# Performance work log

Measured on AMD Instinct MI355X. Metric: run time of the kernel, lower is better.

The kernel has to match this reference:

```python
import jax, jax.numpy as jnp
import numpy as np

N, E, C, EMB, NB, L = 20000, 640000, 64, 32, 8, 2
MAX_RADIUS = 2.5
NUM_NEIGHBORS = 32.0
RH = 32  # radial MLP hidden


def setup_inputs() -> dict:
    key = jax.random.key(0)
    ks = jax.random.split(key, 24)
    g = lambda k, shape, fan: (jax.random.normal(k, shape, dtype=jnp.float32) / np.sqrt(fan).astype(np.float32))
    inp = {
        'x': jax.random.normal(ks[0], (N, 6), dtype=jnp.float32),
        'batch': jnp.zeros((N,), dtype=jnp.int64),
        'node_attr': jax.random.randint(ks[1], (N,), 0, 100),
        'edge_src': jax.random.randint(ks[2], (E,), 0, N),
        'edge_dst': jax.random.randint(ks[3], (E,), 0, N),
        'emb_table': jax.random.normal(ks[4], (100, EMB), dtype=jnp.float32),
        'uplift_M': jax.random.normal(ks[5], (C, 2), dtype=jnp.float32),
        'h': jnp.ones((L,), jnp.float32) * 0.01,
        'mix': jnp.ones((L,), jnp.float32) * 0.5,
        'rad_W1': g(ks[6], (L, NB, RH), NB),
        'rad_b1': jnp.zeros((L, RH), jnp.float32),
        'rad_W2': g(ks[7], (L, RH, 2 * C), RH),
        'lin1_s': g(ks[8], (L, C, C), C),
        'lin1_v': g(ks[9], (L, C, C), C),
        'lin2_s': g(ks[10], (L, C, 2 * C), C),
        'lin2_v': g(ks[11], (L, C, C), C),
        'sc_s_w': g(ks[12], (L, C, EMB, 2 * C), C * EMB),
        'sc_v_w': g(ks[13], (L, C, EMB, C), C * EMB),
        'si_s': g(ks[14], (L, C, C), C),
        'si_v': g(ks[15], (L, C, C), C),
    }
    return inp


def _forward(x, batch, node_attr, edge_src, edge_dst, emb_table, uplift_M, h, mix,
             rad_W1, rad_b1, rad_W2, lin1_s, lin1_v, lin2_s, lin2_v,
             sc_s_w, sc_v_w, si_s, si_v):
    n = x.shape[0]
    emb = emb_table[node_attr]                       # [N, EMB] node embedding
    # semi-unitarize uplift matrix: Q = M (M^T M)^{-1/2} == U V^T
    U, _, Vt = jnp.linalg.svd(uplift_M, full_matrices=False)
    Q = U @ Vt                                       # [C, 2]
    xv = x.reshape(n, 2, 3)
    y_s = jnp.zeros((n, C), x.dtype)                 # hidden scalars start at 0
    y_v = jnp.einsum('nkx,ck->ncx', xv, Q)           # uplift vectors [N,C,3]
    y = (y_s, y_v)
    y_old = y
    nbas = jnp.arange(1, NB + 1, dtype=x.dtype)
    inv_nn = 1.0 / np.sqrt(NUM_NEIGHBORS).astype(np.float32)
    for i in range(L):
        pos = x[:, :3]
        ev = pos[edge_src] - pos[edge_dst]           # [E,3]
        elen = jnp.linalg.norm(ev, axis=1)
        safe = jnp.maximum(elen, 1e-9)
        sh = np.float32(np.sqrt(3.0)) * ev / safe[:, None]   # 1x1o SH, component norm
        # bessel radial basis, scaled by sqrt(NB)
        ef = (np.float32(np.sqrt(2.0 / MAX_RADIUS)) *
              jnp.sin(nbas[None, :] * jnp.pi * safe[:, None] / MAX_RADIUS) / safe[:, None])
        ef = ef * np.float32(np.sqrt(NB))
        # smooth cutoff (e3nn tetris style)
        u = 2.0 * (elen / MAX_RADIUS - 1.0)
        cut = jnp.where(u > 0, 0.0, jnp.where(u < -2, 1.0, 0.5 * (1.0 - jnp.cos(jnp.pi * u))))
        ea = cut[:, None] * sh                       # [E,3] edge attr
        # linear pre-mix
        s1 = y[0] @ lin1_s[i]                        # [N,C]
        v1 = jnp.einsum('ncx,cd->ndx', y[1], lin1_v[i])  # [N,C,3]
        # radial MLP -> per-edge TP weights
        w = jax.nn.silu(ef @ rad_W1[i] + rad_b1[i]) @ rad_W2[i]  # [E,2C]
        w1, w2 = w[:, :C], w[:, C:]
        # tensor-product messages: 0e x 1o -> 1o ; 1o . 1o -> 0e
        msg_v = (w1 * s1[edge_src])[:, :, None] * ea[:, None, :]        # [E,C,3]
        msg_s = w2 * jnp.einsum('ecx,ex->ec', v1[edge_src], ea)         # [E,C]
        agg_s = jax.ops.segment_sum(msg_s, edge_dst, num_segments=n) * inv_nn
        agg_v = jax.ops.segment_sum(msg_v, edge_dst, num_segments=n) * inv_nn
        # post linear + node-attr self connection
        out_s = agg_s @ lin2_s[i] + jnp.einsum('nc,ne,ceo->no', y[0], emb, sc_s_w[i])   # [N,2C]
        out_v = (jnp.einsum('ncx,cd->ndx', agg_v, lin2_v[i]) +
                 jnp.einsum('ncx,ne,ceo->nox', y[1], emb, sc_v_w[i]))                   # [N,C,3]
        # gated nonlinearity
        g_s = jax.nn.silu(out_s[:, :C])
        g_v = jax.nn.sigmoid(out_s[:, C:])[:, :, None] * out_v
        # self interaction
        y2_s = y[0] @ si_s[i]
        y2_v = jnp.einsum('ncx,cd->ndx', y[1], si_v[i])
        # leapfrog update
        hh = h[i] * h[i]
        m = mix[i]
        new_s = 2.0 * y[0] - y_old[0] + hh * (m * g_s + (m - 1.0) * y2_s)
        new_v = 2.0 * y[1] - y_old[1] + hh * (m * g_v + (m - 1.0) * y2_v)
        y_old = y
        y = (new_s, new_v)
        x = jnp.einsum('ncx,ck->nkx', new_v, Q).reshape(n, 6)   # project
    return x


def reference(x, batch, node_attr, edge_src, edge_dst, emb_table, uplift_M, h, mix,
              rad_W1, rad_b1, rad_W2, lin1_s, lin1_v, lin2_s, lin2_v,
              sc_s_w, sc_v_w, si_s, si_v):
    return _forward(x, batch, node_attr, edge_src, edge_dst, emb_table, uplift_M, h, mix,
                    rad_W1, rad_b1, rad_W2, lin1_s, lin1_v, lin2_s, lin2_v,
                    sc_s_w, sc_v_w, si_s, si_v)
```

## Files before the change

### kernel.cpp

```cpp
#include <hip/hip_runtime.h>
#include <cstdio>
#include <cstdint>

#define CCH 64
#define EMBD 32
#define NBD 8
#define RHD 32
#define NATTR 100
#define TBINS 64

static constexpr float MAXR    = 2.5f;
static constexpr float INVNN   = 0.17677669529663687f;
static constexpr float EFK     = 2.5298221281347035f;
static constexpr float SQRT3   = 1.7320508075688772f;
static constexpr float PI_F    = 3.14159265358979323846f;

__device__ __forceinline__ float sigm_(float x) { return 1.f / (1.f + __expf(-x)); }
__device__ __forceinline__ float silu_(float x) { return x / (1.f + __expf(-x)); }
__device__ __forceinline__ unsigned f2bfu(float f) {
    unsigned u = __float_as_uint(f);
    return (u + 0x7FFF + ((u >> 16) & 1)) >> 16;
}
__device__ __forceinline__ unsigned pack2(float lo, float hi) {
    return f2bfu(lo) | (f2bfu(hi) << 16);
}
__device__ __forceinline__ float ulo(unsigned u) { return __uint_as_float(u << 16); }
__device__ __forceinline__ float uhi(unsigned u) { return __uint_as_float(u & 0xFFFF0000u); }

__global__ void kQ(const float* M, float* Q) {
    int c = threadIdx.x;
    float m0 = M[2*c], m1 = M[2*c+1];
    float a = m0*m0, b = m0*m1, d = m1*m1;
    for (int o = 32; o > 0; o >>= 1) {
        a += __shfl_xor(a, o); b += __shfl_xor(b, o); d += __shfl_xor(d, o);
    }
    float det = a*d - b*b;
    float s = sqrtf(det);
    float t = sqrtf(a + d + 2.f*s);
    float inv = 1.f / (s*t);
    float i00 = (d + s)*inv, i01 = -b*inv, i11 = (a + s)*inv;
    Q[2*c]   = m0*i00 + m1*i01;
    Q[2*c+1] = m0*i01 + m1*i11;
}

__global__ void kRadTab(const float* __restrict__ rW1, const float* __restrict__ rb1,
                        const float* __restrict__ rW2, unsigned* __restrict__ tab) {
    int bin = blockIdx.x;
    int l   = blockIdx.y;
    int lane = threadIdx.x;
    float r = bin * (MAXR / TBINS);
    float safe = fmaxf(r, 1e-9f);
    float invSafe = 1.f / safe;
    float th = PI_F * r * (1.f / MAXR);
    float s0, c0;
    __sincosf(th, &s0, &c0);
    __shared__ float hidS[RHD];
    if (lane < RHD) {
        float hs = rb1[l*RHD + lane];
        float sPrev = 0.f, sCur = s0, twoC = 2.f*c0;
        #pragma unroll
        for (int b = 0; b < NBD; ++b) {
            float efb = EFK * sCur * invSafe;
            hs = fmaf(efb, rW1[(l*NBD + b)*RHD + lane], hs);
            float sN = fmaf(twoC, sCur, -sPrev);
            sPrev = sCur; sCur = sN;
        }
        hidS[lane] = silu_(hs);
    }
    __syncthreads();
    float w1 = 0.f, w2 = 0.f;
    #pragma unroll
    for (int rr = 0; rr < RHD; ++rr) {
        float h = hidS[rr];
        w1 = fmaf(h, rW2[(l*RHD + rr)*128 + lane], w1);
        w2 = fmaf(h, rW2[(l*RHD + rr)*128 + 64 + lane], w2);
    }
    float cut = s0*s0;
    float coef = SQRT3 * cut * invSafe;
    tab[((size_t)l*(TBINS+1) + bin)*64 + lane] = pack2(w1*coef, w2*coef);
}

__global__ __launch_bounds__(256) void kInitLin(const float* __restrict__ x, const float* __restrict__ Qg,
        const float* __restrict__ L1v,
        float* __restrict__ yAs, float* __restrict__ yAv, float4* __restrict__ pos4,
        uint2* __restrict__ mv, int n) {
    __shared__ unsigned wPk[32*64];
    __shared__ uint2 bc[4][64];
    int t = threadIdx.x;
    for (int i = t; i < 32*64; i += 256) {
        int cp = i >> 6, o = i & 63;
        wPk[i] = pack2(L1v[(2*cp)*64 + o], L1v[(2*cp+1)*64 + o]);
    }
    __syncthreads();
    int lane = t & 63;
    int wid = t >> 6;
    float q0 = Qg[2*lane], q1 = Qg[2*lane+1];
    for (int node = blockIdx.x*4 + wid; node < n; node += gridDim.x*4) {
        const float* xr = x + (size_t)node*6;
        float x0 = xr[0], x1 = xr[1], x2 = xr[2], x3 = xr[3], x4 = xr[4], x5 = xr[5];
        float y0 = q0*x0 + q1*x3;
        float y1 = q0*x1 + q1*x4;
        float y2 = q0*x2 + q1*x5;
        float* yv = yAv + (size_t)node*192 + lane*3;
        yv[0] = y0; yv[1] = y1; yv[2] = y2;
        yAs[(size_t)node*64 + lane] = 0.f;
        if (lane == 0) pos4[node] = (float4){x0, x1, x2, 0.f};
        bc[wid][lane] = (uint2){ pack2(y0, y1), pack2(y2, 0.f) };
        float a0A=0.f, a0B=0.f, a1A=0.f, a1B=0.f, a2A=0.f, a2B=0.f;
        #pragma unroll 8
        for (int cp = 0; cp < 32; ++cp) {
            int c = 2*cp;
            uint2 b0 = bc[wid][c];
            uint2 b1 = bc[wid][c+1];
            unsigned wp = wPk[cp*64 + lane];
            float wv0 = ulo(wp), wv1 = uhi(wp);
            a0A = fmaf(ulo(b0.x), wv0, a0A); a0B = fmaf(ulo(b1.x), wv1, a0B);
            a1A = fmaf(uhi(b0.x), wv0, a1A); a1B = fmaf(uhi(b1.x), wv1, a1B);
            a2A = fmaf(ulo(b0.y), wv0, a2A); a2B = fmaf(ulo(b1.y), wv1, a2B);
        }
        mv[(size_t)node*64 + lane] =
            (uint2){ pack2(a0A+a0B, a1A+a1B), pack2(a2A+a2B, 0.f) };
    }
}

__global__ void kHist(const int* dst, int* cnt, int e) {
    int i = blockIdx.x*blockDim.x + threadIdx.x;
    if (i < e) atomicAdd(&cnt[dst[i]], 1);
}

__global__ void kScan(const int* cnt, int* offs, int* cursor, int n) {
    __shared__ int part[1024];
    int t = threadIdx.x;
    int chunk = (n + 1023) >> 10;
    int lo = t*chunk, hi = min(lo + chunk, n);
    int s = 0;
    for (int i = lo; i < hi; ++i) s += cnt[i];
    part[t] = s;
    __syncthreads();
    for (int o = 1; o < 1024; o <<= 1) {
        int w = (t >= o) ? part[t - o] : 0;
        __syncthreads();
        part[t] += w;
        __syncthreads();
    }
    int run = part[t] - s;
    for (int i = lo; i < hi; ++i) {
        int cv = cnt[i];
        offs[i] = run; cursor[i] = run;
        run += cv;
    }
    if (t == 1023) offs[n] = part[1023];
}

__global__ void kScatter(const int* src, const int* dst, int* cursor,
                         int* srcSorted, int e) {
    int i = blockIdx.x*blockDim.x + threadIdx.x;
    if (i < e) {
        int p = atomicAdd(&cursor[dst[i]], 1);
        srcSorted[p] = src[i];
    }
}

__global__ __launch_bounds__(256) void kT3(const float* __restrict__ embT,
        const float* __restrict__ scs, const float* __restrict__ scv,
        unsigned* __restrict__ Tsp, unsigned* __restrict__ Tvp) {
    int cp = blockIdx.x, l = blockIdx.y, ag = blockIdx.z;
    int c0 = 2*cp, c1 = c0 + 1;
    __shared__ float sS0[32*128], sS1[32*128], sV0[32*64], sV1[32*64], sE[20*EMBD];
    int t = threadIdx.x;
    const float* p0 = scs + ((size_t)(l*CCH + c0)*EMBD)*128;
    const float* p1 = scs + ((size_t)(l*CCH + c1)*EMBD)*128;
    for (int i = t; i < 32*128; i += 256) { sS0[i] = p0[i]; sS1[i] = p1[i]; }
    const float* q0 = scv + ((size_t)(l*CCH + c0)*EMBD)*64;
    const float* q1 = scv + ((size_t)(l*CCH + c1)*EMBD)*64;
    for (int i = t; i < 32*64; i += 256) { sV0[i] = q0[i]; sV1[i] = q1[i]; }
    const float* eb = embT + (size_t)ag*20*EMBD;
    for (int i = t; i < 20*EMBD; i += 256) sE[i] = eb[i];
    __syncthreads();
    if (t < 128) {
        int o = t;
        for (int a = 0; a < 20; ++a) {
            float acc0 = 0.f, acc1 = 0.f;
            #pragma unroll
            for (int e = 0; e < EMBD; ++e) {
                float ev = sE[a*EMBD + e];
                acc0 = fmaf(ev, sS0[e*128 + o], acc0);
                acc1 = fmaf(ev, sS1[e*128 + o], acc1);
            }
            int aa = ag*20 + a;
            Tsp[(((size_t)l*NATTR + aa)*32 + cp)*128 + o] = pack2(acc0, acc1);
        }
    } else if (t < 192) {
        int o = t - 128;
        for (int a = 0; a < 20; ++a) {
            float acc0 = 0.f, acc1 = 0.f;
            #pragma unroll
            for (int e = 0; e < EMBD; ++e) {
                float ev = sE[a*EMBD + e];
                acc0 = fmaf(ev, sV0[e*64 + o], acc0);
                acc1 = fmaf(ev, sV1[e*64 + o], acc1);
            }
            int aa = ag*20 + a;
            Tvp[(((size_t)l*NATTR + aa)*32 + cp)*64 + o] = pack2(acc0, acc1);
        }
    }
}

__global__ __launch_bounds__(256) void kLin1(const float* __restrict__ ys, const float* __restrict__ yv,
        const float* __restrict__ L1s, const float* __restrict__ L1v,
        uint2* __restrict__ mv, int n) {
    __shared__ uint2 wPk[32*64];
    __shared__ uint2 bc[4][64];
    int t = threadIdx.x;
    for (int i = t; i < 32*64; i += 256) {
        int cp = i >> 6, o = i & 63;
        wPk[i] = (uint2){ pack2(L1s[(2*cp)*64 + o], L1s[(2*cp+1)*64 + o]),
                          pack2(L1v[(2*cp)*64 + o], L1v[(2*cp+1)*64 + o]) };
    }
    __syncthreads();
    int lane = t & 63;
    int wid = t >> 6;
    for (int node = blockIdx.x*4 + wid; node < n; node += gridDim.x*4) {
        float ys_r = ys[(size_t)node*64 + lane];
        const float* yvp = yv + (size_t)node*192 + lane*3;
        float y0 = yvp[0], y1 = yvp[1], y2 = yvp[2];
        bc[wid][lane] = (uint2){ pack2(y0, y1), pack2(y2, ys_r) };
        float asA=0.f, asB=0.f, a0A=0.f, a0B=0.f, a1A=0.f, a1B=0.f, a2A=0.f, a2B=0.f;
        #pragma unroll 8
        for (int cp = 0; cp < 32; ++cp) {
            int c = 2*cp;
            uint2 b0 = bc[wid][c];
            uint2 b1 = bc[wid][c+1];
            uint2 wp = wPk[cp*64 + lane];
            float ws0 = ulo(wp.x), ws1 = uhi(wp.x);
            float wv0 = ulo(wp.y), wv1 = uhi(wp.y);
            asA = fmaf(uhi(b0.y), ws0, asA); asB = fmaf(uhi(b1.y), ws1, asB);
            a0A = fmaf(ulo(b0.x), wv0, a0A); a0B = fmaf(ulo(b1.x), wv1, a0B);
            a1A = fmaf(uhi(b0.x), wv0, a1A); a1B = fmaf(uhi(b1.x), wv1, a1B);
            a2A = fmaf(ulo(b0.y), wv0, a2A); a2B = fmaf(ulo(b1.y), wv1, a2B);
        }
        mv[(size_t)node*64 + lane] =
            (uint2){ pack2(a0A+a0B, a1A+a1B), pack2(a2A+a2B, asA+asB) };
    }
}

template<int WITHV>
__global__ __launch_bounds__(256) void kAgg(const float4* __restrict__ pos4,
        const uint2* __restrict__ mv,
        const int* __restrict__ offs, const int* __restrict__ srcSorted,
        const unsigned* __restrict__ tabG,
        float* __restrict__ aggS, float* __restrict__ aggV, int n) {
    __shared__ unsigned tab[(TBINS+1)*64];
    __shared__ float red[4][64][4];
    int t = threadIdx.x;
    for (int i = t; i < (TBINS+1)*64; i += 256) tab[i] = tabG[i];
    __syncthreads();
    int lane = t & 63;
    int wid = t >> 6;

    for (int node = blockIdx.x; node < n; node += gridDim.x) {
        float4 pc = pos4[node];
        float px = pc.x, py = pc.y, pz = pc.z;
        int beg = offs[node], end = offs[node+1];
        float accS = 0.f, av0 = 0.f, av1 = 0.f, av2 = 0.f;
        int idx = beg + wid;
        int srcA = 0, srcB = 0;
        float4 pA = (float4){0.f,0.f,0.f,0.f};
        if (idx < end) srcA = srcSorted[idx];
        if (idx + 4 < end) srcB = srcSorted[idx + 4];
        if (idx < end) pA = pos4[srcA];
        for (; idx < end; idx += 4) {
            int srcU = srcA;
            float ex = pA.x - px, ey = pA.y - py, ez = pA.z - pz;
            srcA = srcB;
            if (idx + 8 < end) srcB = srcSorted[idx + 8];
            if (idx + 4 < end) pA = pos4[srcA];
            float el2 = ex*ex + ey*ey + ez*ez;
            if (el2 >= MAXR*MAXR) continue;
            uint2 mw = mv[(size_t)srcU*64 + lane];
            float elen = sqrtf(el2);
            float u = elen * ((float)TBINS / MAXR);
            int i0 = (int)u;
            float fr = u - (float)i0;
            unsigned t0 = tab[i0*64 + lane];
            unsigned t1 = tab[i0*64 + 64 + lane];
            float w1 = fmaf(fr, ulo(t1) - ulo(t0), ulo(t0));
            float w2 = fmaf(fr, uhi(t1) - uhi(t0), uhi(t0));
            float vv0 = ulo(mw.x), vv1 = uhi(mw.x), vv2 = ulo(mw.y);
            float dv = vv0*ex + vv1*ey + vv2*ez;
            accS = fmaf(w2, dv, accS);
            if (WITHV) {
                float tt = w1 * uhi(mw.y);
                av0 = fmaf(tt, ex, av0); av1 = fmaf(tt, ey, av1); av2 = fmaf(tt, ez, av2);
            }
        }
        red[wid][lane][0] = accS; red[wid][lane][1] = av0;
        red[wid][lane][2] = av1;  red[wid][lane][3] = av2;
        __syncthreads();
        if (wid == 0) {
            float rs = red[0][lane][0] + red[1][lane][0] + red[2][lane][0] + red[3][lane][0];
            aggS[(size_t)node*64 + lane] = rs*INVNN;
            float r0 = red[0][lane][1] + red[1][lane][1] + red[2][lane][1] + red[3][lane][1];
            float r1 = red[0][lane][2] + red[1][lane][2] + red[2][lane][2] + red[3][lane][2];
            float r2 = red[0][lane][3] + red[1][lane][3] + red[2][lane][3] + red[3][lane][3];
            float* ap = aggV + (size_t)node*192 + lane*3;
            ap[0] = r0*INVNN; ap[1] = r1*INVNN; ap[2] = r2*INVNN;
        }
        __syncthreads();
    }
}

__global__ __launch_bounds__(256) void kOutComb(const float* __restrict__ ys, const float* __restrict__ yv,
        const float* __restrict__ yolds, const float* __restrict__ yoldv,
        const float* __restrict__ aggS, const float* __restrict__ aggV, const int* __restrict__ attr,
        const float* __restrict__ L2s, const float* __restrict__ L2v,
        const unsigned* __restrict__ Tsp, const unsigned* __restrict__ Tvp,
        const float* __restrict__ siS, const float* __restrict__ siV, const float* __restrict__ Qg,
        const float* __restrict__ hArr, const float* __restrict__ mArr, int li,
        float* __restrict__ newS, float* __restrict__ newV,
        float4* __restrict__ pos4out, float* __restrict__ xout6,
        int writeY, int n) {
    __shared__ uint2 wAB[32*64];
    __shared__ uint2 wLS[32*64];
    __shared__ unsigned wSv[32*64];
    __shared__ uint4 bcast[4][64];
    int t = threadIdx.x;
    for (int i = t; i < 32*64; i += 256) {
        int cp = i >> 6, o = i & 63;
        wAB[i] = (uint2){ pack2(L2s[(2*cp)*128 + o],      L2s[(2*cp+1)*128 + o]),
                          pack2(L2s[(2*cp)*128 + 64 + o], L2s[(2*cp+1)*128 + 64 + o]) };
        wLS[i] = (uint2){ pack2(L2v[(2*cp)*64 + o], L2v[(2*cp+1)*64 + o]),
                          pack2(siS[(2*cp)*64 + o], siS[(2*cp+1)*64 + o]) };
        wSv[i] = pack2(siV[(2*cp)*64 + o], siV[(2*cp+1)*64 + o]);
    }
    __syncthreads();
    int lane = t & 63;
    int wid = t >> 6;
    float hh = hArr[li]; hh *= hh;
    float m = mArr[li];
    float q0 = Qg[2*lane], q1 = Qg[2*lane+1];
    for (int node = blockIdx.x*4 + wid; node < n; node += gridDim.x*4) {
        int a = attr[node];
        const unsigned* tS = Tsp + (size_t)a*32*128;
        const unsigned* tV = Tvp + (size_t)a*32*64;
        float as_r = aggS[(size_t)node*64 + lane];
        float ys_r = ys[(size_t)node*64 + lane];
        const float* avp = aggV + (size_t)node*192 + lane*3;
        float av0 = avp[0], av1 = avp[1], av2 = avp[2];
        const float* yvp = yv + (size_t)node*192 + lane*3;
        float by0 = yvp[0], by1 = yvp[1], by2 = yvp[2];
        bcast[wid][lane] = (uint4){ pack2(as_r, ys_r), pack2(av0, by0),
                                    pack2(av1, by1),   pack2(av2, by2) };
        float oS0A=0.f,oS0B=0.f, oS1A=0.f,oS1B=0.f;
        float ov0A=0.f,ov0B=0.f, ov1A=0.f,ov1B=0.f, ov2A=0.f,ov2B=0.f;
        float q2sA=0.f,q2sB=0.f, qv0A=0.f,qv0B=0.f, qv1A=0.f,qv1B=0.f, qv2A=0.f,qv2B=0.f;
        #pragma unroll 4
        for (int cp = 0; cp < 32; ++cp) {
            int c = 2*cp;
            uint4 b0 = bcast[wid][c];
            uint4 b1 = bcast[wid][c+1];
            float asc0 = ulo(b0.x), ysc0 = uhi(b0.x);
            float asc1 = ulo(b1.x), ysc1 = uhi(b1.x);
            float a00 = ulo(b0.y), b00 = uhi(b0.y);
            float a10 = ulo(b1.y), b10 = uhi(b1.y);
            float a01 = ulo(b0.z), b01 = uhi(b0.z);
            float a11 = ulo(b1.z), b11 = uhi(b1.z);
            float a02 = ulo(b0.w), b02 = uhi(b0.w);
            float a12 = ulo(b1.w), b12 = uhi(b1.w);
            uint2 ab = wAB[cp*64 + lane];
            uint2 ls = wLS[cp*64 + lane];
            unsigned sv = wSv[cp*64 + lane];
            unsigned ts0 = tS[cp*128 + lane];
            unsigned ts1 = tS[cp*128 + 64 + lane];
            unsigned tvw = tV[cp*64 + lane];
            float lsa0 = ulo(ab.x), lsa1 = uhi(ab.x);
            float lsb0 = ulo(ab.y), lsb1 = uhi(ab.y);
            float lv0 = ulo(ls.x), lv1 = uhi(ls.x);
            float ws0 = ulo(ls.y), ws1 = uhi(ls.y);
            float wv0 = ulo(sv), wv1 = uhi(sv);
            float tsa0 = ulo(ts0), tsa1 = uhi(ts0);
            float tsb0 = ulo(ts1), tsb1 = uhi(ts1);
            float tv0 = ulo(tvw), tv1 = uhi(tvw);
            oS0A = fmaf(asc0, lsa0, fmaf(ysc0, tsa0, oS0A));
            oS0B = fmaf(asc1, lsa1, fmaf(ysc1, tsa1, oS0B));
            oS1A = fmaf(asc0, lsb0, fmaf(ysc0, tsb0, oS1A));
            oS1B = fmaf(asc1, lsb1, fmaf(ysc1, tsb1, oS1B));
            ov0A = fmaf(a00, lv0, fmaf(b00, tv0, ov0A));
            ov0B = fmaf(a10, lv1, fmaf(b10, tv1, ov0B));
            ov1A = fmaf(a01, lv0, fmaf(b01, tv0, ov1A));
            ov1B = fmaf(a11, lv1, fmaf(b11, tv1, ov1B));
            ov2A = fmaf(a02, lv0, fmaf(b02, tv0, ov2A));
            ov2B = fmaf(a12, lv1, fmaf(b12, tv1, ov2B));
            q2sA = fmaf(ysc0, ws0, q2sA); q2sB = fmaf(ysc1, ws1, q2sB);
            qv0A = fmaf(b00, wv0, qv0A);  qv0B = fmaf(b10, wv1, qv0B);
            qv1A = fmaf(b01, wv0, qv1A);  qv1B = fmaf(b11, wv1, qv1B);
            qv2A = fmaf(b02, wv0, qv2A);  qv2B = fmaf(b12, wv1, qv2B);
        }
        float gs = silu_(oS0A + oS0B);
        float sg = sigm_(oS1A + oS1B);
        float gv0 = sg*(ov0A+ov0B), gv1 = sg*(ov1A+ov1B), gv2 = sg*(ov2A+ov2B);
        float q2s = q2sA+q2sB, qv0 = qv0A+qv0B, qv1 = qv1A+qv1B, qv2 = qv2A+qv2B;
        float yos = yolds[(size_t)node*64 + lane];
        const float* yop = yoldv + (size_t)node*192 + lane*3;
        float ns  = 2.f*ys_r - yos   + hh*(m*gs  + (m-1.f)*q2s);
        float nv0 = 2.f*by0 - yop[0] + hh*(m*gv0 + (m-1.f)*qv0);
        float nv1 = 2.f*by1 - yop[1] + hh*(m*gv1 + (m-1.f)*qv1);
        float nv2 = 2.f*by2 - yop[2] + hh*(m*gv2 + (m-1.f)*qv2);
        if (writeY) {
            newS[(size_t)node*64 + lane] = ns;
            float* np = newV + (size_t)node*192 + lane*3;
            np[0] = nv0; np[1] = nv1; np[2] = nv2;
        }
        float p00 = nv0*q0, p01 = nv1*q0, p02 = nv2*q0;
        float p10 = nv0*q1, p11 = nv1*q1, p12 = nv2*q1;
        for (int o = 32; o > 0; o >>= 1) {
            p00 += __shfl_xor(p00, o); p01 += __shfl_xor(p01, o); p02 += __shfl_xor(p02, o);
            p10 += __shfl_xor(p10, o); p11 += __shfl_xor(p11, o); p12 += __shfl_xor(p12, o);
        }
        if (lane == 0) {
            if (writeY) {
                pos4out[node] = (float4){p00, p01, p02, 0.f};
            } else {
                float* xp = xout6 + (size_t)node*6;
                xp[0] = p00; xp[1] = p01; xp[2] = p02;
                xp[3] = p10; xp[4] = p11; xp[5] = p12;
            }
        }
    }
}

extern "C" void kernel_launch(void* const* d_in, const int* in_sizes, int n_in,
                              void* d_out, int out_size, void* d_ws, size_t ws_size,
                              hipStream_t stream) {
    const float* x        = (const float*)d_in[0];
    const int*   nattr    = (const int*)  d_in[2];
    const int*   esrc     = (const int*)  d_in[3];
    const int*   edst     = (const int*)  d_in[4];
    const float* embT     = (const float*)d_in[5];
    const float* upM      = (const float*)d_in[6];
    const float* hArr     = (const float*)d_in[7];
    const float* mArr     = (const float*)d_in[8];
    const float* rW1      = (const float*)d_in[9];
    const float* rb1      = (const float*)d_in[10];
    const float* rW2      = (const float*)d_in[11];
    const float* l1s      = (const float*)d_in[12];
    const float* l1v      = (const float*)d_in[13];
    const float* l2s      = (const float*)d_in[14];
    const float* l2v      = (const float*)d_in[15];
    const float* scs      = (const float*)d_in[16];
    const float* scv      = (const float*)d_in[17];
    const float* sis      = (const float*)d_in[18];
    const float* siv      = (const float*)d_in[19];
    int n = in_sizes[0] / 6;
    int e = in_sizes[3];
    float* out = (float*)d_out;

    float* w = (float*)d_ws;
    float* Q    = w; w += 128;
    float* yAs  = w; w += (size_t)n*64;
    float* yAv  = w; w += (size_t)n*192;
    float* yBs  = w; w += (size_t)n*64;
    float* yBv  = w; w += (size_t)n*192;
    float* aggS = w; w += (size_t)n*64;
    float* aggV = w; w += (size_t)n*192;
    float4* pos4 = (float4*)w; w += (size_t)n*4;
    uint2* mv    = (uint2*)w;  w += (size_t)n*128;
    unsigned* Tsp = (unsigned*)w; w += (size_t)2*NATTR*32*128;
    unsigned* Tvp = (unsigned*)w; w += (size_t)2*NATTR*32*64;
    unsigned* radTab = (unsigned*)w; w += (size_t)2*(TBINS+1)*64;
    int* cnt       = (int*)w;
    int* offs      = cnt + n;
    int* cursor    = offs + (n + 1);
    int* srcSorted = cursor + n;
    size_t need = (size_t)((char*)(srcSorted + e) - (char*)d_ws);
    if (need > ws_size) {
        fprintf(stderr, "kernel_launch: ws too small (%zu > %zu)\n", need, ws_size);
        return;
    }

    const int AGG_GRID  = 1792;
    const int OC_GRID   = 768;
    const int LIN_GRID  = 2048;

    kQ<<<1, 64, 0, stream>>>(upM, Q);
    hipMemsetAsync(cnt, 0, (size_t)n*sizeof(int), stream);
    kHist<<<(e + 255)/256, 256, 0, stream>>>(edst, cnt, e);
    kScan<<<1, 1024, 0, stream>>>(cnt, offs, cursor, n);
    kScatter<<<(e + 255)/256, 256, 0, stream>>>(esrc, edst, cursor, srcSorted, e);
    kT3<<<dim3(32, 2, 5), 256, 0, stream>>>(embT, scs, scv, Tsp, Tvp);
    kRadTab<<<dim3(TBINS+1, 2), 64, 0, stream>>>(rW1, rb1, rW2, radTab);
    kInitLin<<<LIN_GRID, 256, 0, stream>>>(x, Q, l1v, yAs, yAv, pos4, mv, n);

    kAgg<0><<<AGG_GRID, 256, 0, stream>>>(pos4, mv, offs, srcSorted,
                                  radTab, aggS, aggV, n);
    kOutComb<<<OC_GRID, 256, 0, stream>>>(yAs, yAv, yAs, yAv, aggS, aggV, nattr,
                                  l2s, l2v, Tsp, Tvp, sis, siv, Q, hArr, mArr, 0,
                                  yBs, yBv, pos4, out, 1, n);
    kLin1<<<LIN_GRID, 256, 0, stream>>>(yBs, yBv, l1s + 4096, l1v + 4096, mv, n);
    kAgg<1><<<AGG_GRID, 256, 0, stream>>>(pos4, mv, offs, srcSorted,
                                  radTab + (size_t)(TBINS+1)*64, aggS, aggV, n);
    kOutComb<<<OC_GRID, 256, 0, stream>>>(yBs, yBv, yAs, yAv, aggS, aggV, nattr,
                                  l2s + (size_t)64*128, l2v + (size_t)64*64,
                                  Tsp + (size_t)NATTR*32*128, Tvp + (size_t)NATTR*32*64,
                                  sis + 4096, siv + 4096, Q, hArr, mArr, 1,
                                  yAs, yAv, pos4, out, 0, n);
}
```

Before: 575.0 us.

## Switch node linear layers to packed fp16 dot2 with register-held self-interaction weights

The node-wise linear kernels (kInitLin, kLin1, kOutComb) and the precomputed embedding-contracted tables change from bf16 storage with scalar fp32 FMAs to fp16 packed pairs consumed by v_dot2 instructions. This roughly halves the ALU instruction count and removes the unpack shifts. Broadcast buffers get a channel-pair layout so each step needs one 16-byte LDS read. The siV weights are packed into fp16 by a new kernel and held in 32 registers per thread in kOutComb, and that kernel's grid grows. The cost is fp16 range and precision on activations, plus extra register pressure.

```diff
diff --git a/kernel.cpp b/kernel.cpp
--- a/kernel.cpp
+++ b/kernel.cpp
@@ -15,6 +15,8 @@
 static constexpr float SQRT3   = 1.7320508075688772f;
 static constexpr float PI_F    = 3.14159265358979323846f;
 
+typedef __fp16 v2h __attribute__((ext_vector_type(2)));
+
 __device__ __forceinline__ float sigm_(float x) { return 1.f / (1.f + __expf(-x)); }
 __device__ __forceinline__ float silu_(float x) { return x / (1.f + __expf(-x)); }
 __device__ __forceinline__ unsigned f2bfu(float f) {
@@ -26,6 +28,17 @@
 }
 __device__ __forceinline__ float ulo(unsigned u) { return __uint_as_float(u << 16); }
 __device__ __forceinline__ float uhi(unsigned u) { return __uint_as_float(u & 0xFFFF0000u); }
+__device__ __forceinline__ v2h u2h(unsigned u) { v2h h; __builtin_memcpy(&h, &u, 4); return h; }
+__device__ __forceinline__ unsigned pkh(float a, float b) {
+    v2h h = __builtin_amdgcn_cvt_pkrtz(a, b);
+    unsigned u; __builtin_memcpy(&u, &h, 4); return u;
+}
+__device__ __forceinline__ unsigned short h1(float f) {
+    __fp16 h = (__fp16)f; unsigned short s; __builtin_memcpy(&s, &h, 2); return s;
+}
+__device__ __forceinline__ float dot2(unsigned a, unsigned b, float c) {
+    return __builtin_amdgcn_fdot2(u2h(a), u2h(b), c, false);
+}
 
 __global__ void kQ(const float* M, float* Q) {
     int c = threadIdx.x;
@@ -80,16 +93,23 @@
     tab[((size_t)l*(TBINS+1) + bin)*64 + lane] = pack2(w1*coef, w2*coef);
 }
 
+__global__ void kPackW(const float* __restrict__ siv, unsigned* __restrict__ siVp) {
+    int l = blockIdx.y;
+    int i = blockIdx.x*256 + threadIdx.x;
+    int cp = i >> 6, o = i & 63;
+    siVp[l*2048 + i] = pkh(siv[l*4096 + (2*cp)*64 + o], siv[l*4096 + (2*cp+1)*64 + o]);
+}
+
 __global__ __launch_bounds__(256) void kInitLin(const float* __restrict__ x, const float* __restrict__ Qg,
         const float* __restrict__ L1v,
         float* __restrict__ yAs, float* __restrict__ yAv, float4* __restrict__ pos4,
         uint2* __restrict__ mv, int n) {
     __shared__ unsigned wPk[32*64];
-    __shared__ uint2 bc[4][64];
+    __shared__ __align__(16) unsigned bc[4][32][4];
     int t = threadIdx.x;
     for (int i = t; i < 32*64; i += 256) {
         int cp = i >> 6, o = i & 63;
-        wPk[i] = pack2(L1v[(2*cp)*64 + o], L1v[(2*cp+1)*64 + o]);
+        wPk[i] = pkh(L1v[(2*cp)*64 + o], L1v[(2*cp+1)*64 + o]);
     }
     __syncthreads();
     int lane = t & 63;
@@ -105,21 +125,21 @@
         yv[0] = y0; yv[1] = y1; yv[2] = y2;
         yAs[(size_t)node*64 + lane] = 0.f;
         if (lane == 0) pos4[node] = (float4){x0, x1, x2, 0.f};
-        bc[wid][lane] = (uint2){ pack2(y0, y1), pack2(y2, 0.f) };
-        float a0A=0.f, a0B=0.f, a1A=0.f, a1B=0.f, a2A=0.f, a2B=0.f;
+        {
+            unsigned short* p = (unsigned short*)bc[wid][lane >> 1];
+            int sub = lane & 1;
+            p[0*2+sub] = h1(y0); p[1*2+sub] = h1(y1); p[2*2+sub] = h1(y2);
+        }
+        float a0 = 0.f, a1 = 0.f, a2 = 0.f;
         #pragma unroll 8
         for (int cp = 0; cp < 32; ++cp) {
-            int c = 2*cp;
-            uint2 b0 = bc[wid][c];
-            uint2 b1 = bc[wid][c+1];
+            uint4 b = *(const uint4*)&bc[wid][cp][0];
             unsigned wp = wPk[cp*64 + lane];
-            float wv0 = ulo(wp), wv1 = uhi(wp);
-            a0A = fmaf(ulo(b0.x), wv0, a0A); a0B = fmaf(ulo(b1.x), wv1, a0B);
-            a1A = fmaf(uhi(b0.x), wv0, a1A); a1B = fmaf(uhi(b1.x), wv1, a1B);
-            a2A = fmaf(ulo(b0.y), wv0, a2A); a2B = fmaf(ulo(b1.y), wv1, a2B);
-        }
-        mv[(size_t)node*64 + lane] =
-            (uint2){ pack2(a0A+a0B, a1A+a1B), pack2(a2A+a2B, 0.f) };
+            a0 = dot2(b.x, wp, a0);
+            a1 = dot2(b.y, wp, a1);
+            a2 = dot2(b.z, wp, a2);
+        }
+        mv[(size_t)node*64 + lane] = (uint2){ pack2(a0, a1), pack2(a2, 0.f) };
     }
 }
 
@@ -188,7 +208,7 @@
                 acc1 = fmaf(ev, sS1[e*128 + o], acc1);
             }
             int aa = ag*20 + a;
-            Tsp[(((size_t)l*NATTR + aa)*32 + cp)*128 + o] = pack2(acc0, acc1);
+            Tsp[((size_t)(l*NATTR + aa)*32 + cp)*128 + (o & 63)*2 + (o >> 6)] = pkh(acc0, acc1);
         }
     } else if (t < 192) {
         int o = t - 128;
@@ -201,7 +221,7 @@
                 acc1 = fmaf(ev, sV1[e*64 + o], acc1);
             }
             int aa = ag*20 + a;
-            Tvp[(((size_t)l*NATTR + aa)*32 + cp)*64 + o] = pack2(acc0, acc1);
+            Tvp[((size_t)(l*NATTR + aa)*32 + cp)*64 + o] = pkh(acc0, acc1);
         }
     }
 }
@@ -210,12 +230,12 @@
         const float* __restrict__ L1s, const float* __restrict__ L1v,
         uint2* __restrict__ mv, int n) {
     __shared__ uint2 wPk[32*64];
-    __shared__ uint2 bc[4][64];
+    __shared__ __align__(16) unsigned bc[4][32][4];
     int t = threadIdx.x;
     for (int i = t; i < 32*64; i += 256) {
         int cp = i >> 6, o = i & 63;
-        wPk[i] = (uint2){ pack2(L1s[(2*cp)*64 + o], L1s[(2*cp+1)*64 + o]),
-                          pack2(L1v[(2*cp)*64 + o], L1v[(2*cp+1)*64 + o]) };
+        wPk[i] = (uint2){ pkh(L1s[(2*cp)*64 + o], L1s[(2*cp+1)*64 + o]),
+                          pkh(L1v[(2*cp)*64 + o], L1v[(2*cp+1)*64 + o]) };
     }
     __syncthreads();
     int lane = t & 63;
@@ -224,23 +244,23 @@
         float ys_r = ys[(size_t)node*64 + lane];
         const float* yvp = yv + (size_t)node*192 + lane*3;
         float y0 = yvp[0], y1 = yvp[1], y2 = yvp[2];
-        bc[wid][lane] = (uint2){ pack2(y0, y1), pack2(y2, ys_r) };
-        float asA=0.f, asB=0.f, a0A=0.f, a0B=0.f, a1A=0.f, a1B=0.f, a2A=0.f, a2B=0.f;
+        {
+            unsigned short* p = (unsigned short*)bc[wid][lane >> 1];
+            int sub = lane & 1;
+            p[0*2+sub] = h1(y0); p[1*2+sub] = h1(y1);
+            p[2*2+sub] = h1(y2); p[3*2+sub] = h1(ys_r);
+        }
+        float as = 0.f, a0 = 0.f, a1 = 0.f, a2 = 0.f;
         #pragma unroll 8
         for (int cp = 0; cp < 32; ++cp) {
-            int c = 2*cp;
-            uint2 b0 = bc[wid][c];
-            uint2 b1 = bc[wid][c+1];
+            uint4 b = *(const uint4*)&bc[wid][cp][0];
             uint2 wp = wPk[cp*64 + lane];
-            float ws0 = ulo(wp.x), ws1 = uhi(wp.x);
-            float wv0 = ulo(wp.y), wv1 = uhi(wp.y);
-            asA = fmaf(uhi(b0.y), ws0, asA); asB = fmaf(uhi(b1.y), ws1, asB);
-            a0A = fmaf(ulo(b0.x), wv0, a0A); a0B = fmaf(ulo(b1.x), wv1, a0B);
-            a1A = fmaf(uhi(b0.x), wv0, a1A); a1B = fmaf(uhi(b1.x), wv1, a1B);
-            a2A = fmaf(ulo(b0.y), wv0, a2A); a2B = fmaf(ulo(b1.y), wv1, a2B);
-        }
-        mv[(size_t)node*64 + lane] =
-            (uint2){ pack2(a0A+a0B, a1A+a1B), pack2(a2A+a2B, asA+asB) };
+            as = dot2(b.w, wp.x, as);
+            a0 = dot2(b.x, wp.y, a0);
+            a1 = dot2(b.y, wp.y, a1);
+            a2 = dot2(b.z, wp.y, a2);
+        }
+        mv[(size_t)node*64 + lane] = (uint2){ pack2(a0, a1), pack2(a2, as) };
     }
 }
 
@@ -315,27 +335,28 @@
         const float* __restrict__ aggS, const float* __restrict__ aggV, const int* __restrict__ attr,
         const float* __restrict__ L2s, const float* __restrict__ L2v,
         const unsigned* __restrict__ Tsp, const unsigned* __restrict__ Tvp,
-        const float* __restrict__ siS, const float* __restrict__ siV, const float* __restrict__ Qg,
+        const float* __restrict__ siS, const unsigned* __restrict__ siVp, const float* __restrict__ Qg,
         const float* __restrict__ hArr, const float* __restrict__ mArr, int li,
         float* __restrict__ newS, float* __restrict__ newV,
         float4* __restrict__ pos4out, float* __restrict__ xout6,
         int writeY, int n) {
     __shared__ uint2 wAB[32*64];
     __shared__ uint2 wLS[32*64];
-    __shared__ unsigned wSv[32*64];
-    __shared__ uint4 bcast[4][64];
+    __shared__ __align__(16) unsigned bc[4][32][8];
     int t = threadIdx.x;
     for (int i = t; i < 32*64; i += 256) {
         int cp = i >> 6, o = i & 63;
-        wAB[i] = (uint2){ pack2(L2s[(2*cp)*128 + o],      L2s[(2*cp+1)*128 + o]),
-                          pack2(L2s[(2*cp)*128 + 64 + o], L2s[(2*cp+1)*128 + 64 + o]) };
-        wLS[i] = (uint2){ pack2(L2v[(2*cp)*64 + o], L2v[(2*cp+1)*64 + o]),
-                          pack2(siS[(2*cp)*64 + o], siS[(2*cp+1)*64 + o]) };
-        wSv[i] = pack2(siV[(2*cp)*64 + o], siV[(2*cp+1)*64 + o]);
+        wAB[i] = (uint2){ pkh(L2s[(2*cp)*128 + o],      L2s[(2*cp+1)*128 + o]),
+                          pkh(L2s[(2*cp)*128 + 64 + o], L2s[(2*cp+1)*128 + 64 + o]) };
+        wLS[i] = (uint2){ pkh(L2v[(2*cp)*64 + o], L2v[(2*cp+1)*64 + o]),
+                          pkh(siS[(2*cp)*64 + o], siS[(2*cp+1)*64 + o]) };
     }
     __syncthreads();
     int lane = t & 63;
     int wid = t >> 6;
+    unsigned svr[32];
+    #pragma unroll
+    for (int cp = 0; cp < 32; ++cp) svr[cp] = siVp[cp*64 + lane];
     float hh = hArr[li]; hh *= hh;
     float m = mArr[li];
     float q0 = Qg[2*lane], q1 = Qg[2*lane+1];
@@ -349,57 +370,37 @@
         float av0 = avp[0], av1 = avp[1], av2 = avp[2];
         const float* yvp = yv + (size_t)node*192 + lane*3;
         float by0 = yvp[0], by1 = yvp[1], by2 = yvp[2];
-        bcast[wid][lane] = (uint4){ pack2(as_r, ys_r), pack2(av0, by0),
-                                    pack2(av1, by1),   pack2(av2, by2) };
-        float oS0A=0.f,oS0B=0.f, oS1A=0.f,oS1B=0.f;
-        float ov0A=0.f,ov0B=0.f, ov1A=0.f,ov1B=0.f, ov2A=0.f,ov2B=0.f;
-        float q2sA=0.f,q2sB=0.f, qv0A=0.f,qv0B=0.f, qv1A=0.f,qv1B=0.f, qv2A=0.f,qv2B=0.f;
+        {
+            unsigned short* p = (unsigned short*)bc[wid][lane >> 1];
+            int sub = lane & 1;
+            p[0*2+sub] = h1(as_r); p[1*2+sub] = h1(ys_r);
+            p[2*2+sub] = h1(av0);  p[3*2+sub] = h1(by0);
+            p[4*2+sub] = h1(av1);  p[5*2+sub] = h1(by1);
+            p[6*2+sub] = h1(av2);  p[7*2+sub] = h1(by2);
+        }
+        float oS0=0.f, oS1=0.f, ov0=0.f, ov1=0.f, ov2=0.f;
+        float q2s=0.f, qv0=0.f, qv1=0.f, qv2=0.f;
         #pragma unroll 4
         for (int cp = 0; cp < 32; ++cp) {
-            int c = 2*cp;
-            uint4 b0 = bcast[wid][c];
-            uint4 b1 = bcast[wid][c+1];
-            float asc0 = ulo(b0.x), ysc0 = uhi(b0.x);
-            float asc1 = ulo(b1.x), ysc1 = uhi(b1.x);
-            float a00 = ulo(b0.y), b00 = uhi(b0.y);
-            float a10 = ulo(b1.y), b10 = uhi(b1.y);
-            float a01 = ulo(b0.z), b01 = uhi(b0.z);
-            float a11 = ulo(b1.z), b11 = uhi(b1.z);
-            float a02 = ulo(b0.w), b02 = uhi(b0.w);
-            float a12 = ulo(b1.w), b12 = uhi(b1.w);
+            uint4 bA = *(const uint4*)&bc[wid][cp][0];
+            uint4 bB = *(const uint4*)&bc[wid][cp][4];
             uint2 ab = wAB[cp*64 + lane];
             uint2 ls = wLS[cp*64 + lane];
-            unsigned sv = wSv[cp*64 + lane];
-            unsigned ts0 = tS[cp*128 + lane];
-            unsigned ts1 = tS[cp*128 + 64 + lane];
-            unsigned tvw = tV[cp*64 + lane];
-            float lsa0 = ulo(ab.x), lsa1 = uhi(ab.x);
-            float lsb0 = ulo(ab.y), lsb1 = uhi(ab.y);
-            float lv0 = ulo(ls.x), lv1 = uhi(ls.x);
-            float ws0 = ulo(ls.y), ws1 = uhi(ls.y);
-            float wv0 = ulo(sv), wv1 = uhi(sv);
-            float tsa0 = ulo(ts0), tsa1 = uhi(ts0);
-            float tsb0 = ulo(ts1), tsb1 = uhi(ts1);
-            float tv0 = ulo(tvw), tv1 = uhi(tvw);
-            oS0A = fmaf(asc0, lsa0, fmaf(ysc0, tsa0, oS0A));
-            oS0B = fmaf(asc1, lsa1, fmaf(ysc1, tsa1, oS0B));
-            oS1A = fmaf(asc0, lsb0, fmaf(ysc0, tsb0, oS1A));
-            oS1B = fmaf(asc1, lsb1, fmaf(ysc1, tsb1, oS1B));
-            ov0A = fmaf(a00, lv0, fmaf(b00, tv0, ov0A));
-            ov0B = fmaf(a10, lv1, fmaf(b10, tv1, ov0B));
-            ov1A = fmaf(a01, lv0, fmaf(b01, tv0, ov1A));
-            ov1B = fmaf(a11, lv1, fmaf(b11, tv1, ov1B));
-            ov2A = fmaf(a02, lv0, fmaf(b02, tv0, ov2A));
-            ov2B = fmaf(a12, lv1, fmaf(b12, tv1, ov2B));
-            q2sA = fmaf(ysc0, ws0, q2sA); q2sB = fmaf(ysc1, ws1, q2sB);
-            qv0A = fmaf(b00, wv0, qv0A);  qv0B = fmaf(b10, wv1, qv0B);
-            qv1A = fmaf(b01, wv0, qv1A);  qv1B = fmaf(b11, wv1, qv1B);
-            qv2A = fmaf(b02, wv0, qv2A);  qv2B = fmaf(b12, wv1, qv2B);
-        }
-        float gs = silu_(oS0A + oS0B);
-        float sg = sigm_(oS1A + oS1B);
-        float gv0 = sg*(ov0A+ov0B), gv1 = sg*(ov1A+ov1B), gv2 = sg*(ov2A+ov2B);
-        float q2s = q2sA+q2sB, qv0 = qv0A+qv0B, qv1 = qv1A+qv1B, qv2 = qv2A+qv2B;
+            uint2 ts = *(const uint2*)&tS[(cp*64 + lane)*2];
+            unsigned tv = tV[cp*64 + lane];
+            oS0 = dot2(bA.x, ab.x, dot2(bA.y, ts.x, oS0));
+            oS1 = dot2(bA.x, ab.y, dot2(bA.y, ts.y, oS1));
+            ov0 = dot2(bA.z, ls.x, dot2(bA.w, tv, ov0));
+            ov1 = dot2(bB.x, ls.x, dot2(bB.y, tv, ov1));
+            ov2 = dot2(bB.z, ls.x, dot2(bB.w, tv, ov2));
+            q2s = dot2(bA.y, ls.y, q2s);
+            qv0 = dot2(bA.w, svr[cp], qv0);
+            qv1 = dot2(bB.y, svr[cp], qv1);
+            qv2 = dot2(bB.w, svr[cp], qv2);
+        }
+        float gs = silu_(oS0);
+        float sg = sigm_(oS1);
+        float gv0 = sg*ov0, gv1 = sg*ov1, gv2 = sg*ov2;
         float yos = yolds[(size_t)node*64 + lane];
         const float* yop = yoldv + (size_t)node*192 + lane*3;
         float ns  = 2.f*ys_r - yos   + hh*(m*gs  + (m-1.f)*q2s);
@@ -468,6 +469,7 @@
     unsigned* Tsp = (unsigned*)w; w += (size_t)2*NATTR*32*128;
     unsigned* Tvp = (unsigned*)w; w += (size_t)2*NATTR*32*64;
     unsigned* radTab = (unsigned*)w; w += (size_t)2*(TBINS+1)*64;
+    unsigned* siVp = (unsigned*)w; w += (size_t)2*2048;
     int* cnt       = (int*)w;
     int* offs      = cnt + n;
     int* cursor    = offs + (n + 1);
@@ -479,7 +481,7 @@
     }
 
     const int AGG_GRID  = 1792;
-    const int OC_GRID   = 768;
+    const int OC_GRID   = 1024;
     const int LIN_GRID  = 2048;
 
     kQ<<<1, 64, 0, stream>>>(upM, Q);
@@ -489,12 +491,13 @@
     kScatter<<<(e + 255)/256, 256, 0, stream>>>(esrc, edst, cursor, srcSorted, e);
     kT3<<<dim3(32, 2, 5), 256, 0, stream>>>(embT, scs, scv, Tsp, Tvp);
     kRadTab<<<dim3(TBINS+1, 2), 64, 0, stream>>>(rW1, rb1, rW2, radTab);
+    kPackW<<<dim3(8, 2), 256, 0, stream>>>(siv, siVp);
     kInitLin<<<LIN_GRID, 256, 0, stream>>>(x, Q, l1v, yAs, yAv, pos4, mv, n);
 
     kAgg<0><<<AGG_GRID, 256, 0, stream>>>(pos4, mv, offs, srcSorted,
                                   radTab, aggS, aggV, n);
     kOutComb<<<OC_GRID, 256, 0, stream>>>(yAs, yAv, yAs, yAv, aggS, aggV, nattr,
-                                  l2s, l2v, Tsp, Tvp, sis, siv, Q, hArr, mArr, 0,
+                                  l2s, l2v, Tsp, Tvp, sis, siVp, Q, hArr, mArr, 0,
                                   yBs, yBv, pos4, out, 1, n);
     kLin1<<<LIN_GRID, 256, 0, stream>>>(yBs, yBv, l1s + 4096, l1v + 4096, mv, n);
     kAgg<1><<<AGG_GRID, 256, 0, stream>>>(pos4, mv, offs, srcSorted,
@@ -502,6 +505,6 @@
     kOutComb<<<OC_GRID, 256, 0, stream>>>(yBs, yBv, yAs, yAv, aggS, aggV, nattr,
                                   l2s + (size_t)64*128, l2v + (size_t)64*64,
                                   Tsp + (size_t)NATTR*32*128, Tvp + (size_t)NATTR*32*64,
-                                  sis + 4096, siv + 4096, Q, hArr, mArr, 1,
+                                  sis + 4096, siVp + 2048, Q, hArr, mArr, 1,
                                   yAs, yAv, pos4, out, 0, n);
 }
```

Measured after the change: 516.3 us. 10.2% less time.
